# Kernel tuning notes

Hardware: AMD Instinct MI355X
Metric: run time of the kernel (lower is better)

The kernel has to match this reference:

```python
import jax, jax.numpy as jnp
import numpy as np

N = 100000      # nodes
E = 1200000     # edges (avg degree ~12)
F_IN = 64       # input feature dim
HID = 64        # hidden_channels
OUT = 64        # out_channels


def setup_inputs() -> dict:
    key = jax.random.key(0)
    ks = jax.random.split(key, 9)
    s_in = 1.0 / np.sqrt(F_IN)
    s_h = 1.0 / np.sqrt(HID)
    inp = {
        "x": jax.random.normal(ks[0], (N, F_IN), dtype=jnp.float32),
        "edge_index": jax.random.randint(ks[1], (2, E), 0, N, dtype=jnp.int64),
        # conv_in: lin_l (with bias) applied to aggregated msgs, lin_r (no bias) to self
        "Wl_in": jax.random.normal(ks[2], (HID, F_IN), dtype=jnp.float32) * s_in,
        "bl_in": jnp.zeros((HID,), dtype=jnp.float32),
        "Wr_in": jax.random.normal(ks[3], (HID, F_IN), dtype=jnp.float32) * s_in,
        # conv_med (shared across the 2 middle applications)
        "Wl_med": jax.random.normal(ks[4], (HID, HID), dtype=jnp.float32) * s_h,
        "bl_med": jnp.zeros((HID,), dtype=jnp.float32),
        "Wr_med": jax.random.normal(ks[5], (HID, HID), dtype=jnp.float32) * s_h,
        # conv_out
        "Wl_out": jax.random.normal(ks[6], (OUT, HID), dtype=jnp.float32) * s_h,
        "bl_out": jnp.zeros((OUT,), dtype=jnp.float32),
        "Wr_out": jax.random.normal(ks[7], (OUT, HID), dtype=jnp.float32) * s_h,
    }
    return inp


def reference(x, edge_index, Wl_in, bl_in, Wr_in, Wl_med, bl_med, Wr_med,
              Wl_out, bl_out, Wr_out):
    src = edge_index[0]
    dst = edge_index[1]
    n = x.shape[0]

    def sage(h, Wl, bl, Wr):
        # sum-aggregate neighbor messages h_j into each destination node i
        agg = jax.ops.segment_sum(h[src], dst, num_segments=n)  # [N, F]
        return agg @ Wl.T + bl + h @ Wr.T

    # eval mode: dropout is identity
    h = jnp.tanh(sage(x, Wl_in, bl_in, Wr_in))
    for _ in range(2):  # conv_med applied twice with shared weights
        h = jnp.tanh(sage(h, Wl_med, bl_med, Wr_med))
    return sage(h, Wl_out, bl_out, Wr_out)
```

## Files before the change

kernel.cpp:

```cpp
#include <hip/hip_runtime.h>
#include <cstdint>

#define F 64
#define TILE1 8192
#define MAXFB 1024
#define SCAN_BLK 1024

typedef short bf16x8 __attribute__((ext_vector_type(8)));
typedef float f32x4  __attribute__((ext_vector_type(4)));

__device__ __forceinline__ unsigned short f2b(float f) {
    unsigned u = __float_as_uint(f);
    unsigned r = u + 0x7fffu + ((u >> 16) & 1u);
    return (unsigned short)(r >> 16);
}
__device__ __forceinline__ void add8(float* a, uint4 u) {
    const unsigned* p = (const unsigned*)&u;
#pragma unroll
    for (int i = 0; i < 4; ++i) {
        a[2 * i + 0] += __uint_as_float(p[i] << 16);
        a[2 * i + 1] += __uint_as_float(p[i] & 0xffff0000u);
    }
}

__global__ __launch_bounds__(256) void prep_hist_kernel(
    const float* __restrict__ Wl0, const float* __restrict__ Wr0,
    const float* __restrict__ Wl1, const float* __restrict__ Wr1,
    const float* __restrict__ Wl2, const float* __restrict__ Wr2,
    ushort* __restrict__ wbuf,
    const float* __restrict__ x, ushort* __restrict__ xb, int nElem,
    const int* __restrict__ dst, int* __restrict__ binMat,
    int E, int NB1, int nf) {
    __shared__ int h[MAXFB];
    int b = blockIdx.x;
    int t = threadIdx.x;
    if (b < 12) {
        int g = b * 256 + t;
        int set = g >> 10;
        int fl = g & 1023;
        int f = fl >> 6;
        int l = fl & 63;
        int s = f >> 2;
        int ot = f & 3;
        const float* Wl = (set == 0) ? Wl0 : (set == 1) ? Wl1 : Wl2;
        const float* Wr = (set == 0) ? Wr0 : (set == 1) ? Wr1 : Wr2;
        int o = ot * 16 + (l & 15);
        int k0 = s * 32 + (l >> 4) * 8;
        unsigned d[4];
#pragma unroll
        for (int p = 0; p < 4; ++p) {
            int ka = k0 + 2 * p, kb = k0 + 2 * p + 1;
            float va = (ka < 64) ? Wl[o * 64 + ka] : Wr[o * 64 + (ka - 64)];
            float vb = (kb < 64) ? Wl[o * 64 + kb] : Wr[o * 64 + (kb - 64)];
            d[p] = (unsigned)f2b(va) | ((unsigned)f2b(vb) << 16);
        }
        ((uint4*)wbuf)[g] = make_uint4(d[0], d[1], d[2], d[3]);
    } else if (b < 12 + NB1) {
        int tb = b - 12;
        for (int i = t; i < nf; i += 256) h[i] = 0;
        __syncthreads();
        int base = tb * TILE1;
        int end = min(base + TILE1, E);
        const int4* d4 = (const int4*)dst;
        int n4 = (end - base) >> 2;
        int b4 = base >> 2;
        for (int k = t; k < n4; k += 256) {
            int4 v = d4[b4 + k];
            atomicAdd(&h[v.x >> 7], 1);
            atomicAdd(&h[v.y >> 7], 1);
            atomicAdd(&h[v.z >> 7], 1);
            atomicAdd(&h[v.w >> 7], 1);
        }
        __syncthreads();
        for (int i = t; i < nf; i += 256) binMat[i * NB1 + tb] = h[i];
    } else {
        int i = (b - 12 - NB1) * 256 + t;
        int n4 = nElem >> 2;
        if (i < n4) {
            float4 v = ((const float4*)x)[i];
            uint2 o;
            o.x = (unsigned)f2b(v.x) | ((unsigned)f2b(v.y) << 16);
            o.y = (unsigned)f2b(v.z) | ((unsigned)f2b(v.w) << 16);
            ((uint2*)xb)[i] = o;
        }
    }
}

__global__ __launch_bounds__(SCAN_BLK) void scan_blocks_kernel(
    int* __restrict__ a, int* __restrict__ blockSums, int len) {
    __shared__ int sh[SCAN_BLK];
    int t = threadIdx.x;
    int i = blockIdx.x * SCAN_BLK + t;
    int v = (i < len) ? a[i] : 0;
    sh[t] = v;
    __syncthreads();
    for (int off = 1; off < SCAN_BLK; off <<= 1) {
        int add = (t >= off) ? sh[t - off] : 0;
        __syncthreads();
        sh[t] += add;
        __syncthreads();
    }
    int incl = sh[t];
    if (i < len) a[i] = incl - v;
    if (t == SCAN_BLK - 1) blockSums[blockIdx.x] = incl;
}

__device__ __forceinline__ void scan_sums_lds(
    const int* __restrict__ blockSums, int nbScan, int* sBS) {
    int t = threadIdx.x;
    int v = (t < nbScan) ? blockSums[t] : 0;
    sBS[t] = v;
    __syncthreads();
    for (int off = 1; off < 256; off <<= 1) {
        int add = (t >= off) ? sBS[t - off] : 0;
        __syncthreads();
        sBS[t] += add;
        __syncthreads();
    }
    int excl = sBS[t] - v;
    __syncthreads();
    sBS[t] = excl;
    __syncthreads();
}

__global__ __launch_bounds__(256) void scatter_kernel(
    const int* __restrict__ src, const int* __restrict__ dst,
    const int* __restrict__ binMat, const int* __restrict__ blockSums,
    unsigned* __restrict__ stage2, int E, int NB1, int nf, int nbScan) {
    __shared__ int cur[MAXFB];
    __shared__ int sBS[256];
    int t = threadIdx.x;
    scan_sums_lds(blockSums, nbScan, sBS);
    for (int i = t; i < nf; i += 256) {
        int j = i * NB1 + blockIdx.x;
        cur[i] = binMat[j] + sBS[j >> 10];
    }
    __syncthreads();
    int base = blockIdx.x * TILE1;
    int end = min(base + TILE1, E);
    const int4* s4 = (const int4*)src;
    const int4* d4 = (const int4*)dst;
    int n4 = (end - base) >> 2;
    int b4 = base >> 2;
    for (int k = t; k < n4; k += 256) {
        int4 s = s4[b4 + k];
        int4 d = d4[b4 + k];
        int p0 = atomicAdd(&cur[d.x >> 7], 1);
        int p1 = atomicAdd(&cur[d.y >> 7], 1);
        int p2 = atomicAdd(&cur[d.z >> 7], 1);
        int p3 = atomicAdd(&cur[d.w >> 7], 1);
        stage2[p0] = ((unsigned)(d.x & 127) << 17) | (unsigned)s.x;
        stage2[p1] = ((unsigned)(d.y & 127) << 17) | (unsigned)s.y;
        stage2[p2] = ((unsigned)(d.z & 127) << 17) | (unsigned)s.z;
        stage2[p3] = ((unsigned)(d.w & 127) << 17) | (unsigned)s.w;
    }
}

__global__ __launch_bounds__(256) void phase2_kernel(
    const unsigned* __restrict__ stage2, const int* __restrict__ binMat,
    const int* __restrict__ blockSums,
    int* __restrict__ csrSrc, int* __restrict__ rowStart,
    int E, int NB1, int nf, int nbScan) {
    __shared__ int cnt[128];
    __shared__ int pre[129];
    __shared__ int cur[128];
    __shared__ int sBS[256];
    int b = blockIdx.x;
    int t = threadIdx.x;
    scan_sums_lds(blockSums, nbScan, sBS);
    int j0 = b * NB1;
    int s = binMat[j0] + sBS[j0 >> 10];
    int e2 = E;
    if (b + 1 < nf) {
        int j1 = (b + 1) * NB1;
        e2 = binMat[j1] + sBS[j1 >> 10];
    }
    if (t < 128) cnt[t] = 0;
    __syncthreads();
    for (int i = s + t; i < e2; i += 256)
        atomicAdd(&cnt[(stage2[i] >> 17) & 127], 1);
    __syncthreads();
    if (t < 128) pre[t + 1] = cnt[t];
    if (t == 0) pre[0] = 0;
    __syncthreads();
    for (int off = 1; off < 128; off <<= 1) {
        int v = 0;
        if (t < 128 && (t + 1) > off) v = pre[t + 1 - off];
        __syncthreads();
        if (t < 128 && (t + 1) > off) pre[t + 1] += v;
        __syncthreads();
    }
    if (t < 128) cur[t] = pre[t];
    if (t < 129) rowStart[b * 128 + t] = s + pre[t];
    __syncthreads();
    for (int i = s + t; i < e2; i += 256) {
        unsigned w = stage2[i];
        int pos = atomicAdd(&cur[(w >> 17) & 127], 1);
        csrSrc[s + pos] = (int)(w & 0x1FFFFu);
    }
}

__global__ __launch_bounds__(512, 4) void fused_layer(
    const ushort* __restrict__ hb, const int* __restrict__ rowStart,
    const int* __restrict__ csrSrc, const ushort* __restrict__ wbuf,
    const float* __restrict__ bl, void* __restrict__ out, int n, int flags) {
    __shared__ __align__(16) ushort smem[128 * 72];

    int t = threadIdx.x;
    int node0b = blockIdx.x * 128;
    const uint4* h16 = (const uint4*)hb;

    {
        int c2 = (t & 3) * 2;
        int nl = t >> 2;
        int node = node0b + nl;
        float a[16];
#pragma unroll
        for (int i = 0; i < 16; ++i) a[i] = 0.f;
        int e = rowStart[node];
        int end = rowStart[node + 1];
        for (; e + 3 < end; e += 4) {
            int s0 = csrSrc[e + 0];
            int s1 = csrSrc[e + 1];
            int s2 = csrSrc[e + 2];
            int s3 = csrSrc[e + 3];
            uint4 u0a = h16[(size_t)s0 * 8 + c2], u0b = h16[(size_t)s0 * 8 + c2 + 1];
            uint4 u1a = h16[(size_t)s1 * 8 + c2], u1b = h16[(size_t)s1 * 8 + c2 + 1];
            uint4 u2a = h16[(size_t)s2 * 8 + c2], u2b = h16[(size_t)s2 * 8 + c2 + 1];
            uint4 u3a = h16[(size_t)s3 * 8 + c2], u3b = h16[(size_t)s3 * 8 + c2 + 1];
            add8(a, u0a); add8(a + 8, u0b);
            add8(a, u1a); add8(a + 8, u1b);
            add8(a, u2a); add8(a + 8, u2b);
            add8(a, u3a); add8(a + 8, u3b);
        }
        for (; e < end; ++e) {
            int s0 = csrSrc[e];
            uint4 ua = h16[(size_t)s0 * 8 + c2], ub = h16[(size_t)s0 * 8 + c2 + 1];
            add8(a, ua); add8(a + 8, ub);
        }
        unsigned d[8];
#pragma unroll
        for (int p = 0; p < 8; ++p)
            d[p] = (unsigned)f2b(a[2 * p]) | ((unsigned)f2b(a[2 * p + 1]) << 16);
        uint4* dp = (uint4*)(smem + nl * 72 + c2 * 8);
        dp[0] = make_uint4(d[0], d[1], d[2], d[3]);
        dp[1] = make_uint4(d[4], d[5], d[6], d[7]);
    }
    __syncthreads();

    int w = t >> 6;
    int l = t & 63;
    int quad = l >> 4;
    int lo = l & 15;

    f32x4 acc[4];
#pragma unroll
    for (int ot = 0; ot < 4; ++ot) {
        float bv = bl[ot * 16 + lo];
        f32x4 bvv = {bv, bv, bv, bv};
        acc[ot] = bvv;
    }

#pragma unroll
    for (int s = 0; s < 4; ++s) {
        bf16x8 A;
        if (s < 2) {
            int nl = w * 16 + lo;
            A = *(const bf16x8*)(smem + nl * 72 + s * 32 + quad * 8);
        } else {
            size_t node = (size_t)node0b + w * 16 + lo;
            A = *(const bf16x8*)(hb + node * 64 + (s & 1) * 32 + quad * 8);
        }
#pragma unroll
        for (int ot = 0; ot < 4; ++ot) {
            bf16x8 B = *(const bf16x8*)(wbuf + (((s * 4 + ot) * 64) + l) * 8);
            acc[ot] = __builtin_amdgcn_mfma_f32_16x16x32_bf16(A, B, acc[ot], 0, 0, 0);
        }
    }
    __syncthreads();

    float* outT = (float*)smem;
    int whalf = w >> 2;
    int wrow = (w & 3) * 16;

#pragma unroll
    for (int half = 0; half < 2; ++half) {
        if (whalf == half) {
#pragma unroll
            for (int ot = 0; ot < 4; ++ot) {
                f32x4 v = acc[ot];
                if (flags & 1) {
                    v[0] = tanhf(v[0]); v[1] = tanhf(v[1]);
                    v[2] = tanhf(v[2]); v[3] = tanhf(v[3]);
                }
                int row = wrow + quad * 4;
                int col = ot * 16 + lo;
#pragma unroll
                for (int r = 0; r < 4; ++r)
                    outT[(row + r) * 68 + col] = v[r];
            }
        }
        __syncthreads();
        int hr = t >> 3;
        int node = node0b + half * 64 + hr;
        if (node < n) {
            const float* srcp = &outT[hr * 68 + (t & 7) * 8];
            if (flags & 2) {
                uint4* o8 = (uint4*)out;
                unsigned dd[4];
#pragma unroll
                for (int p = 0; p < 4; ++p) {
                    float va = srcp[2 * p];
                    float vb = srcp[2 * p + 1];
                    dd[p] = (unsigned)f2b(va) | ((unsigned)f2b(vb) << 16);
                }
                o8[(size_t)node * 8 + (t & 7)] = make_uint4(dd[0], dd[1], dd[2], dd[3]);
            } else {
                float4* o16 = (float4*)out;
#pragma unroll
                for (int q = 0; q < 2; ++q) {
                    float4 v = *(const float4*)(srcp + q * 4);
                    o16[(size_t)node * 16 + (t & 7) * 2 + q] = v;
                }
            }
        }
        if (half == 0) __syncthreads();
    }
}

extern "C" void kernel_launch(void* const* d_in, const int* in_sizes, int n_in,
                              void* d_out, int out_size, void* d_ws, size_t ws_size,
                              hipStream_t stream) {
    const float* x      = (const float*)d_in[0];
    const int*   edges  = (const int*)d_in[1];
    const float* Wl_in  = (const float*)d_in[2];
    const float* bl_in  = (const float*)d_in[3];
    const float* Wr_in  = (const float*)d_in[4];
    const float* Wl_med = (const float*)d_in[5];
    const float* bl_med = (const float*)d_in[6];
    const float* Wr_med = (const float*)d_in[7];
    const float* Wl_out = (const float*)d_in[8];
    const float* bl_out = (const float*)d_in[9];
    const float* Wr_out = (const float*)d_in[10];

    const int N = in_sizes[0] / F;
    const int E = in_sizes[1] / 2;
    const int* src = edges;
    const int* dst = edges + E;

    const int nf  = (N + 127) >> 7;
    const int NB1 = (E + TILE1 - 1) / TILE1;
    const int NR  = nf * 128;
    const int scanLen = nf * NB1;
    const int nbScan = (scanLen + SCAN_BLK - 1) / SCAN_BLK;

    ushort*  wbuf      = (ushort*)d_ws;
    ushort*  xb        = wbuf + 3 * 8192;
    ushort*  hAb       = xb + (size_t)NR * F;
    ushort*  hBb       = hAb + (size_t)NR * F;
    int*     rowStart  = (int*)(hBb + (size_t)NR * F);
    int*     blockSums = rowStart + NR + 2;
    int*     binMat    = blockSums + SCAN_BLK;
    unsigned* stage2   = (unsigned*)(binMat + scanLen);
    int*     csrSrc    = (int*)(stage2 + E);

    const int prep_blocks = 12 + NB1 + (N * F / 4 + 255) / 256;

    prep_hist_kernel<<<prep_blocks, 256, 0, stream>>>(
        Wl_in, Wr_in, Wl_med, Wr_med, Wl_out, Wr_out, wbuf, x, xb, N * F,
        dst, binMat, E, NB1, nf);
    scan_blocks_kernel<<<nbScan, SCAN_BLK, 0, stream>>>(binMat, blockSums, scanLen);
    scatter_kernel<<<NB1, 256, 0, stream>>>(src, dst, binMat, blockSums, stage2, E, NB1, nf, nbScan);
    phase2_kernel<<<nf, 256, 0, stream>>>(stage2, binMat, blockSums, csrSrc, rowStart, E, NB1, nf, nbScan);

    fused_layer<<<nf, 512, 0, stream>>>(xb,  rowStart, csrSrc, wbuf,         bl_in,  hAb,   N, 3);
    fused_layer<<<nf, 512, 0, stream>>>(hAb, rowStart, csrSrc, wbuf + 8192,  bl_med, hBb,   N, 3);
    fused_layer<<<nf, 512, 0, stream>>>(hBb, rowStart, csrSrc, wbuf + 8192,  bl_med, hAb,   N, 3);
    fused_layer<<<nf, 512, 0, stream>>>(hAb, rowStart, csrSrc, wbuf + 16384, bl_out, d_out, N, 0);
}
```

Measured before the change: 282.1 us.

## Degree-sort nodes per tile and balance gather work across threads

The CSR build now ranks the 128 nodes of each tile by in-degree and stores that permutation. In the fused layer, each node's gather is handled by 8 threads of 8 features each instead of 4 threads of 16. Each thread group processes one heavy node and one light node (rank i and 127-i) so per-thread edge counts even out, which aims to cut wavefront divergence and tail latency in the aggregation. The cost is an O(128^2) rank computation per tile in phase2, an extra perm buffer read, and a less unrolled per-thread loop.

```diff
diff --git a/kernel.cpp b/kernel.cpp
--- a/kernel.cpp
+++ b/kernel.cpp
@@ -160,11 +160,13 @@
     const unsigned* __restrict__ stage2, const int* __restrict__ binMat,
     const int* __restrict__ blockSums,
     int* __restrict__ csrSrc, int* __restrict__ rowStart,
+    int* __restrict__ perm,
     int E, int NB1, int nf, int nbScan) {
     __shared__ int cnt[128];
     __shared__ int pre[129];
     __shared__ int cur[128];
     __shared__ int sBS[256];
+    __shared__ int permL[128];
     int b = blockIdx.x;
     int t = threadIdx.x;
     scan_sums_lds(blockSums, nbScan, sBS);
@@ -182,6 +184,15 @@
     __syncthreads();
     if (t < 128) pre[t + 1] = cnt[t];
     if (t == 0) pre[0] = 0;
+    if (t < 128) {
+        int my = cnt[t];
+        int r = 0;
+        for (int j = 0; j < 128; ++j) {
+            int cj = cnt[j];
+            r += (cj > my) || (cj == my && j < t);
+        }
+        permL[r] = t;
+    }
     __syncthreads();
     for (int off = 1; off < 128; off <<= 1) {
         int v = 0;
@@ -192,6 +203,7 @@
     }
     if (t < 128) cur[t] = pre[t];
     if (t < 129) rowStart[b * 128 + t] = s + pre[t];
+    if (t < 128) perm[b * 128 + t] = permL[t];
     __syncthreads();
     for (int i = s + t; i < e2; i += 256) {
         unsigned w = stage2[i];
@@ -202,7 +214,8 @@
 
 __global__ __launch_bounds__(512, 4) void fused_layer(
     const ushort* __restrict__ hb, const int* __restrict__ rowStart,
-    const int* __restrict__ csrSrc, const ushort* __restrict__ wbuf,
+    const int* __restrict__ csrSrc, const int* __restrict__ perm,
+    const ushort* __restrict__ wbuf,
     const float* __restrict__ bl, void* __restrict__ out, int n, int flags) {
     __shared__ __align__(16) ushort smem[128 * 72];
 
@@ -211,40 +224,39 @@
     const uint4* h16 = (const uint4*)hb;
 
     {
-        int c2 = (t & 3) * 2;
-        int nl = t >> 2;
-        int node = node0b + nl;
-        float a[16];
-#pragma unroll
-        for (int i = 0; i < 16; ++i) a[i] = 0.f;
-        int e = rowStart[node];
-        int end = rowStart[node + 1];
-        for (; e + 3 < end; e += 4) {
-            int s0 = csrSrc[e + 0];
-            int s1 = csrSrc[e + 1];
-            int s2 = csrSrc[e + 2];
-            int s3 = csrSrc[e + 3];
-            uint4 u0a = h16[(size_t)s0 * 8 + c2], u0b = h16[(size_t)s0 * 8 + c2 + 1];
-            uint4 u1a = h16[(size_t)s1 * 8 + c2], u1b = h16[(size_t)s1 * 8 + c2 + 1];
-            uint4 u2a = h16[(size_t)s2 * 8 + c2], u2b = h16[(size_t)s2 * 8 + c2 + 1];
-            uint4 u3a = h16[(size_t)s3 * 8 + c2], u3b = h16[(size_t)s3 * 8 + c2 + 1];
-            add8(a, u0a); add8(a + 8, u0b);
-            add8(a, u1a); add8(a + 8, u1b);
-            add8(a, u2a); add8(a + 8, u2b);
-            add8(a, u3a); add8(a + 8, u3b);
-        }
-        for (; e < end; ++e) {
-            int s0 = csrSrc[e];
-            uint4 ua = h16[(size_t)s0 * 8 + c2], ub = h16[(size_t)s0 * 8 + c2 + 1];
-            add8(a, ua); add8(a + 8, ub);
-        }
-        unsigned d[8];
-#pragma unroll
-        for (int p = 0; p < 8; ++p)
-            d[p] = (unsigned)f2b(a[2 * p]) | ((unsigned)f2b(a[2 * p + 1]) << 16);
-        uint4* dp = (uint4*)(smem + nl * 72 + c2 * 8);
-        dp[0] = make_uint4(d[0], d[1], d[2], d[3]);
-        dp[1] = make_uint4(d[4], d[5], d[6], d[7]);
+        int c = t & 7;
+        int tm = t >> 3;
+        const int* permB = perm + blockIdx.x * 128;
+        int nl0 = permB[tm];
+        int nl1 = permB[127 - tm];
+#pragma unroll 1
+        for (int r = 0; r < 2; ++r) {
+            int nl = (r == 0) ? nl0 : nl1;
+            int node = node0b + nl;
+            float a[8] = {0.f, 0.f, 0.f, 0.f, 0.f, 0.f, 0.f, 0.f};
+            int e = rowStart[node];
+            int end = rowStart[node + 1];
+            for (; e + 3 < end; e += 4) {
+                int s0 = csrSrc[e + 0];
+                int s1 = csrSrc[e + 1];
+                int s2 = csrSrc[e + 2];
+                int s3 = csrSrc[e + 3];
+                uint4 u0 = h16[(size_t)s0 * 8 + c];
+                uint4 u1 = h16[(size_t)s1 * 8 + c];
+                uint4 u2 = h16[(size_t)s2 * 8 + c];
+                uint4 u3 = h16[(size_t)s3 * 8 + c];
+                add8(a, u0); add8(a, u1); add8(a, u2); add8(a, u3);
+            }
+            for (; e < end; ++e) {
+                uint4 u0 = h16[(size_t)csrSrc[e] * 8 + c];
+                add8(a, u0);
+            }
+            unsigned d[4];
+#pragma unroll
+            for (int p = 0; p < 4; ++p)
+                d[p] = (unsigned)f2b(a[2 * p]) | ((unsigned)f2b(a[2 * p + 1]) << 16);
+            *(uint4*)(smem + nl * 72 + c * 8) = make_uint4(d[0], d[1], d[2], d[3]);
+        }
     }
     __syncthreads();
 
@@ -363,6 +375,7 @@
     int*     binMat    = blockSums + SCAN_BLK;
     unsigned* stage2   = (unsigned*)(binMat + scanLen);
     int*     csrSrc    = (int*)(stage2 + E);
+    int*     perm      = csrSrc + E;
 
     const int prep_blocks = 12 + NB1 + (N * F / 4 + 255) / 256;
 
@@ -371,10 +384,10 @@
         dst, binMat, E, NB1, nf);
     scan_blocks_kernel<<<nbScan, SCAN_BLK, 0, stream>>>(binMat, blockSums, scanLen);
     scatter_kernel<<<NB1, 256, 0, stream>>>(src, dst, binMat, blockSums, stage2, E, NB1, nf, nbScan);
-    phase2_kernel<<<nf, 256, 0, stream>>>(stage2, binMat, blockSums, csrSrc, rowStart, E, NB1, nf, nbScan);
-
-    fused_layer<<<nf, 512, 0, stream>>>(xb,  rowStart, csrSrc, wbuf,         bl_in,  hAb,   N, 3);
-    fused_layer<<<nf, 512, 0, stream>>>(hAb, rowStart, csrSrc, wbuf + 8192,  bl_med, hBb,   N, 3);
-    fused_layer<<<nf, 512, 0, stream>>>(hBb, rowStart, csrSrc, wbuf + 8192,  bl_med, hAb,   N, 3);
-    fused_layer<<<nf, 512, 0, stream>>>(hAb, rowStart, csrSrc, wbuf + 16384, bl_out, d_out, N, 0);
-}
+    phase2_kernel<<<nf, 256, 0, stream>>>(stage2, binMat, blockSums, csrSrc, rowStart, perm, E, NB1, nf, nbScan);
+
+    fused_layer<<<nf, 512, 0, stream>>>(xb,  rowStart, csrSrc, perm, wbuf,         bl_in,  hAb,   N, 3);
+    fused_layer<<<nf, 512, 0, stream>>>(hAb, rowStart, csrSrc, perm, wbuf + 8192,  bl_med, hBb,   N, 3);
+    fused_layer<<<nf, 512, 0, stream>>>(hBb, rowStart, csrSrc, perm, wbuf + 8192,  bl_med, hAb,   N, 3);
+    fused_layer<<<nf, 512, 0, stream>>>(hAb, rowStart, csrSrc, perm, wbuf + 16384, bl_out, d_out, N, 0);
+}
```

After: 259.0 us. -8.2%, faster.
